# Performance work log

Measured on AMD Instinct MI355X. Metric: run time of the kernel, lower is better.

The kernel has to match this reference:

```python
import jax, jax.numpy as jnp
import numpy as np


def setup_inputs() -> dict:
    key = jax.random.key(0)
    k1, k2 = jax.random.split(key)
    x = jax.random.normal(k1, (65536, 256), dtype=jnp.float32)
    w = jax.random.normal(k2, (256, 1024), dtype=jnp.float32)
    return {"x": x, "w": w}


def reference(x, w):
    # out[b, u] = sum_f (x[b, f] - w[f, u])^2
    x_sq = jnp.sum(x * x, axis=1, keepdims=True)          # [B, 1]
    w_sq = jnp.sum(w * w, axis=0, keepdims=True)          # [1, U]
    cross = jnp.matmul(x, w)                               # [B, U]
    return x_sq - 2.0 * cross + w_sq
```

## Files before the change

### kernel.cpp

```cpp
#include <hip/hip_runtime.h>
#include <stdint.h>

#define M_DIM 65536
#define N_DIM 1024
#define K_DIM 256
#define BM 128
#define BN 128
#define BK 64

typedef __attribute__((ext_vector_type(8))) short short8;
typedef __attribute__((ext_vector_type(8))) unsigned short ushort8;
typedef __attribute__((ext_vector_type(16))) float float16;

__device__ __forceinline__ unsigned short f2bf(float f) {
    unsigned u = __builtin_bit_cast(unsigned, f);
    u += 0x7FFFu + ((u >> 16) & 1u);
    return (unsigned short)(u >> 16);
}

__global__ void prep_w(const float* __restrict__ w,
                       unsigned short* __restrict__ wT,
                       float* __restrict__ w_sq) {
    const int n = blockIdx.x * 256 + threadIdx.x;
    float sq = 0.f;
    for (int kc = 0; kc < 4; ++kc) {
        for (int c = 0; c < 8; ++c) {
            ushort8 pk;
            #pragma unroll
            for (int j = 0; j < 8; ++j) {
                float v = w[(size_t)(kc * 64 + c * 8 + j) * N_DIM + n];
                sq += v * v;
                pk[j] = f2bf(-2.0f * v);
            }
            *(ushort8*)(&wT[kc * 65536 + n * 64 + ((c ^ (n & 7)) << 3)]) = pk;
        }
    }
    w_sq[n] = sq;
}

__global__ __launch_bounds__(256, 3)
void gemm_rbf(const float* __restrict__ x,
              const unsigned short* __restrict__ wT,
              const float* __restrict__ w_sq,
              float* __restrict__ out) {
    __shared__ unsigned short xs[BM * BK];
    __shared__ unsigned short ws[BN * BK];
    __shared__ float xsq_p[16][132];
    __shared__ float xsq[BM];

    const int tid  = threadIdx.x;
    const int lane = tid & 63;
    const int wave = tid >> 6;
    const int wy = wave >> 1, wx = wave & 1;
    const int l31 = lane & 31;
    const int lhi = lane >> 5;
    const int bid = blockIdx.x;
    const int m0 = (bid >> 3) * BM;
    const int n0 = (bid & 7) * BN;

    float16 acc[2][2];
    #pragma unroll
    for (int ty = 0; ty < 2; ++ty)
        #pragma unroll
        for (int tx = 0; tx < 2; ++tx)
            #pragma unroll
            for (int i = 0; i < 16; ++i) acc[ty][tx][i] = 0.f;

    float xpart[8];
    #pragma unroll
    for (int p = 0; p < 8; ++p) xpart[p] = 0.f;

    const int xr = tid >> 4;
    const int xc = tid & 15;

    for (int kt = 0; kt < 4; ++kt) {
        __syncthreads();
        {
            const uint4* __restrict__ src = (const uint4*)(wT + (size_t)kt * 65536 + (size_t)n0 * 64);
            uint4* dst = (uint4*)ws;
            #pragma unroll
            for (int i = 0; i < 4; ++i) dst[tid * 4 + i] = src[tid * 4 + i];
        }
        {
            #pragma unroll
            for (int p = 0; p < 8; ++p) {
                const int r = xr + p * 16;
                const float4 v = *(const float4*)(x + (size_t)(m0 + r) * K_DIM + kt * BK + xc * 4);
                xpart[p] += v.x * v.x + v.y * v.y + v.z * v.z + v.w * v.w;
                uint2 pk;
                pk.x = (unsigned)f2bf(v.x) | ((unsigned)f2bf(v.y) << 16);
                pk.y = (unsigned)f2bf(v.z) | ((unsigned)f2bf(v.w) << 16);
                char* dst = (char*)xs + r * 128 + (((xc >> 1) ^ (r & 7)) << 4) + ((xc & 1) << 3);
                *(uint2*)dst = pk;
            }
        }
        __syncthreads();
        const int arow0 = wy * 64 + l31;
        const int bcol0 = wx * 64 + l31;
        #pragma unroll
        for (int ks = 0; ks < 4; ++ks) {
            const int c = ks * 2 + lhi;
            short8 a[2], b[2];
            #pragma unroll
            for (int ty = 0; ty < 2; ++ty) {
                const int r = arow0 + ty * 32;
                a[ty] = *(const short8*)((const char*)xs + r * 128 + ((c ^ (r & 7)) << 4));
            }
            #pragma unroll
            for (int tx = 0; tx < 2; ++tx) {
                const int cc = bcol0 + tx * 32;
                b[tx] = *(const short8*)((const char*)ws + cc * 128 + ((c ^ (cc & 7)) << 4));
            }
            #pragma unroll
            for (int ty = 0; ty < 2; ++ty)
                #pragma unroll
                for (int tx = 0; tx < 2; ++tx)
                    acc[ty][tx] = __builtin_amdgcn_mfma_f32_32x32x16_bf16(
                        a[ty], b[tx], acc[ty][tx], 0, 0, 0);
        }
    }

    #pragma unroll
    for (int p = 0; p < 8; ++p) xsq_p[xc][xr + p * 16] = xpart[p];
    __syncthreads();
    if (tid < BM) {
        float s = 0.f;
        #pragma unroll
        for (int c = 0; c < 16; ++c) s += xsq_p[c][tid];
        xsq[tid] = s;
    }
    __syncthreads();

    float wsqv[2];
    #pragma unroll
    for (int tx = 0; tx < 2; ++tx) wsqv[tx] = w_sq[n0 + wx * 64 + tx * 32 + l31];

    #pragma unroll
    for (int ty = 0; ty < 2; ++ty) {
        const int rbase = wy * 64 + ty * 32 + 4 * lhi;
        float xv[16];
        #pragma unroll
        for (int i = 0; i < 16; ++i) xv[i] = xsq[rbase + (i & 3) + 8 * (i >> 2)];
        #pragma unroll
        for (int tx = 0; tx < 2; ++tx) {
            const int col = n0 + wx * 64 + tx * 32 + l31;
            #pragma unroll
            for (int i = 0; i < 16; ++i) {
                const int row = m0 + rbase + (i & 3) + 8 * (i >> 2);
                out[(size_t)row * N_DIM + col] = xv[i] + acc[ty][tx][i] + wsqv[tx];
            }
        }
    }
}

__global__ void fallback_k(const float* __restrict__ x, const float* __restrict__ w,
                           float* __restrict__ out) {
    __shared__ float xrow[K_DIM];
    const int b = blockIdx.x;
    xrow[threadIdx.x] = x[(size_t)b * K_DIM + threadIdx.x];
    __syncthreads();
    for (int g = 0; g < 4; ++g) {
        const int u = g * 256 + threadIdx.x;
        float s = 0.f;
        for (int k = 0; k < K_DIM; ++k) {
            const float d = xrow[k] - w[(size_t)k * N_DIM + u];
            s += d * d;
        }
        out[(size_t)b * N_DIM + u] = s;
    }
}

extern "C" void kernel_launch(void* const* d_in, const int* in_sizes, int n_in,
                              void* d_out, int out_size, void* d_ws, size_t ws_size,
                              hipStream_t stream) {
    const float* x = (const float*)d_in[0];
    const float* w = (const float*)d_in[1];
    float* out = (float*)d_out;

    const size_t wT_bytes = (size_t)4 * 1024 * 64 * 2;
    const size_t need = wT_bytes + N_DIM * sizeof(float);
    if (ws_size < need) {
        fallback_k<<<M_DIM, 256, 0, stream>>>(x, w, out);
        return;
    }
    unsigned short* wT = (unsigned short*)d_ws;
    float* w_sq = (float*)((char*)d_ws + wT_bytes);

    prep_w<<<4, 256, 0, stream>>>(w, wT, w_sq);
    gemm_rbf<<<(M_DIM / BM) * (N_DIM / BN), 256, 0, stream>>>(x, wT, w_sq, out);
}
```

Measured before the change: 475.6 us.

## Fuse weight prep into GEMM, prefetch x tiles, and remap blocks per XCD

Removes the separate prep_w kernel. Each GEMM block now loads fp32 w directly, converts it to bf16 scaled by -2, and computes the w column norms in-kernel. The x tile for the next k-step is prefetched into registers while the current one is processed, and the x-norm reduction uses wave shuffles instead of shared memory. The block index is remapped so consecutive blocks on an XCD share m rows. This removes one launch and the serialized prep kernel, at the cost of redundant w conversion in each of the many blocks and higher register pressure.

```diff
diff --git a/kernel.cpp b/kernel.cpp
--- a/kernel.cpp
+++ b/kernel.cpp
@@ -9,44 +9,22 @@
 #define BK 64
 
 typedef __attribute__((ext_vector_type(8))) short short8;
-typedef __attribute__((ext_vector_type(8))) unsigned short ushort8;
 typedef __attribute__((ext_vector_type(16))) float float16;
 
-__device__ __forceinline__ unsigned short f2bf(float f) {
+__device__ __forceinline__ unsigned f2bf(float f) {
     unsigned u = __builtin_bit_cast(unsigned, f);
     u += 0x7FFFu + ((u >> 16) & 1u);
-    return (unsigned short)(u >> 16);
-}
-
-__global__ void prep_w(const float* __restrict__ w,
-                       unsigned short* __restrict__ wT,
-                       float* __restrict__ w_sq) {
-    const int n = blockIdx.x * 256 + threadIdx.x;
-    float sq = 0.f;
-    for (int kc = 0; kc < 4; ++kc) {
-        for (int c = 0; c < 8; ++c) {
-            ushort8 pk;
-            #pragma unroll
-            for (int j = 0; j < 8; ++j) {
-                float v = w[(size_t)(kc * 64 + c * 8 + j) * N_DIM + n];
-                sq += v * v;
-                pk[j] = f2bf(-2.0f * v);
-            }
-            *(ushort8*)(&wT[kc * 65536 + n * 64 + ((c ^ (n & 7)) << 3)]) = pk;
-        }
-    }
-    w_sq[n] = sq;
+    return u >> 16;
 }
 
 __global__ __launch_bounds__(256, 3)
 void gemm_rbf(const float* __restrict__ x,
-              const unsigned short* __restrict__ wT,
-              const float* __restrict__ w_sq,
+              const float* __restrict__ w,
               float* __restrict__ out) {
     __shared__ unsigned short xs[BM * BK];
     __shared__ unsigned short ws[BN * BK];
-    __shared__ float xsq_p[16][132];
     __shared__ float xsq[BM];
+    __shared__ float wsq_p[2][BN];
 
     const int tid  = threadIdx.x;
     const int lane = tid & 63;
@@ -54,9 +32,12 @@
     const int wy = wave >> 1, wx = wave & 1;
     const int l31 = lane & 31;
     const int lhi = lane >> 5;
+
     const int bid = blockIdx.x;
-    const int m0 = (bid >> 3) * BM;
-    const int n0 = (bid & 7) * BN;
+    const int xcd = bid & 7;
+    const int idx = bid >> 3;
+    const int n0 = (idx & 7) * BN;
+    const int m0 = ((xcd << 6) + (idx >> 3)) * BM;
 
     float16 acc[2][2];
     #pragma unroll
@@ -69,32 +50,59 @@
     float xpart[8];
     #pragma unroll
     for (int p = 0; p < 8; ++p) xpart[p] = 0.f;
+    float wsq_r = 0.f;
 
     const int xr = tid >> 4;
     const int xc = tid & 15;
+    const int wcol = tid & 127;
+    const int wkh  = tid >> 7;
+
+    float4 xv[8];
+    #pragma unroll
+    for (int p = 0; p < 8; ++p)
+        xv[p] = *(const float4*)(x + (size_t)(m0 + xr + p * 16) * K_DIM + xc * 4);
 
     for (int kt = 0; kt < 4; ++kt) {
+        float wv[4][8];
+        #pragma unroll
+        for (int c = 0; c < 4; ++c)
+            #pragma unroll
+            for (int j = 0; j < 8; ++j)
+                wv[c][j] = w[(size_t)(kt * BK + wkh * 32 + c * 8 + j) * N_DIM + n0 + wcol];
+
         __syncthreads();
-        {
-            const uint4* __restrict__ src = (const uint4*)(wT + (size_t)kt * 65536 + (size_t)n0 * 64);
-            uint4* dst = (uint4*)ws;
+
+        #pragma unroll
+        for (int p = 0; p < 8; ++p) {
+            const int r = xr + p * 16;
+            const float4 v = xv[p];
+            xpart[p] += v.x * v.x + v.y * v.y + v.z * v.z + v.w * v.w;
+            uint2 pk;
+            pk.x = f2bf(v.x) | (f2bf(v.y) << 16);
+            pk.y = f2bf(v.z) | (f2bf(v.w) << 16);
+            *(uint2*)((char*)xs + r * 128 + (((xc >> 1) ^ (r & 7)) << 4) + ((xc & 1) << 3)) = pk;
+        }
+
+        if (kt < 3) {
             #pragma unroll
-            for (int i = 0; i < 4; ++i) dst[tid * 4 + i] = src[tid * 4 + i];
+            for (int p = 0; p < 8; ++p)
+                xv[p] = *(const float4*)(x + (size_t)(m0 + xr + p * 16) * K_DIM + (kt + 1) * BK + xc * 4);
         }
-        {
+
+        #pragma unroll
+        for (int c = 0; c < 4; ++c) {
+            short8 pk;
             #pragma unroll
-            for (int p = 0; p < 8; ++p) {
-                const int r = xr + p * 16;
-                const float4 v = *(const float4*)(x + (size_t)(m0 + r) * K_DIM + kt * BK + xc * 4);
-                xpart[p] += v.x * v.x + v.y * v.y + v.z * v.z + v.w * v.w;
-                uint2 pk;
-                pk.x = (unsigned)f2bf(v.x) | ((unsigned)f2bf(v.y) << 16);
-                pk.y = (unsigned)f2bf(v.z) | ((unsigned)f2bf(v.w) << 16);
-                char* dst = (char*)xs + r * 128 + (((xc >> 1) ^ (r & 7)) << 4) + ((xc & 1) << 3);
-                *(uint2*)dst = pk;
+            for (int j = 0; j < 8; ++j) {
+                const float v = wv[c][j];
+                wsq_r += v * v;
+                pk[j] = (short)f2bf(-2.0f * v);
             }
+            *(short8*)((char*)ws + wcol * 128 + (((wkh * 4 + c) ^ (wcol & 7)) << 4)) = pk;
         }
+
         __syncthreads();
+
         const int arow0 = wy * 64 + l31;
         const int bcol0 = wx * 64 + l31;
         #pragma unroll
@@ -121,52 +129,39 @@
     }
 
     #pragma unroll
-    for (int p = 0; p < 8; ++p) xsq_p[xc][xr + p * 16] = xpart[p];
-    __syncthreads();
-    if (tid < BM) {
-        float s = 0.f;
-        #pragma unroll
-        for (int c = 0; c < 16; ++c) s += xsq_p[c][tid];
-        xsq[tid] = s;
+    for (int p = 0; p < 8; ++p) {
+        float s = xpart[p];
+        s += __shfl_xor(s, 1);
+        s += __shfl_xor(s, 2);
+        s += __shfl_xor(s, 4);
+        s += __shfl_xor(s, 8);
+        if (xc == 0) xsq[xr + p * 16] = s;
     }
+    wsq_p[wkh][wcol] = wsq_r;
     __syncthreads();
 
     float wsqv[2];
     #pragma unroll
-    for (int tx = 0; tx < 2; ++tx) wsqv[tx] = w_sq[n0 + wx * 64 + tx * 32 + l31];
+    for (int tx = 0; tx < 2; ++tx) {
+        const int c = wx * 64 + tx * 32 + l31;
+        wsqv[tx] = wsq_p[0][c] + wsq_p[1][c];
+    }
 
     #pragma unroll
     for (int ty = 0; ty < 2; ++ty) {
         const int rbase = wy * 64 + ty * 32 + 4 * lhi;
-        float xv[16];
+        float xvv[16];
         #pragma unroll
-        for (int i = 0; i < 16; ++i) xv[i] = xsq[rbase + (i & 3) + 8 * (i >> 2)];
+        for (int i = 0; i < 16; ++i) xvv[i] = xsq[rbase + (i & 3) + 8 * (i >> 2)];
         #pragma unroll
         for (int tx = 0; tx < 2; ++tx) {
             const int col = n0 + wx * 64 + tx * 32 + l31;
             #pragma unroll
             for (int i = 0; i < 16; ++i) {
                 const int row = m0 + rbase + (i & 3) + 8 * (i >> 2);
-                out[(size_t)row * N_DIM + col] = xv[i] + acc[ty][tx][i] + wsqv[tx];
+                out[(size_t)row * N_DIM + col] = xvv[i] + acc[ty][tx][i] + wsqv[tx];
             }
         }
-    }
-}
-
-__global__ void fallback_k(const float* __restrict__ x, const float* __restrict__ w,
-                           float* __restrict__ out) {
-    __shared__ float xrow[K_DIM];
-    const int b = blockIdx.x;
-    xrow[threadIdx.x] = x[(size_t)b * K_DIM + threadIdx.x];
-    __syncthreads();
-    for (int g = 0; g < 4; ++g) {
-        const int u = g * 256 + threadIdx.x;
-        float s = 0.f;
-        for (int k = 0; k < K_DIM; ++k) {
-            const float d = xrow[k] - w[(size_t)k * N_DIM + u];
-            s += d * d;
-        }
-        out[(size_t)b * N_DIM + u] = s;
     }
 }
 
@@ -176,16 +171,7 @@
     const float* x = (const float*)d_in[0];
     const float* w = (const float*)d_in[1];
     float* out = (float*)d_out;
+    (void)d_ws; (void)ws_size;
 
-    const size_t wT_bytes = (size_t)4 * 1024 * 64 * 2;
-    const size_t need = wT_bytes + N_DIM * sizeof(float);
-    if (ws_size < need) {
-        fallback_k<<<M_DIM, 256, 0, stream>>>(x, w, out);
-        return;
-    }
-    unsigned short* wT = (unsigned short*)d_ws;
-    float* w_sq = (float*)((char*)d_ws + wT_bytes);
-
-    prep_w<<<4, 256, 0, stream>>>(w, wT, w_sq);
-    gemm_rbf<<<(M_DIM / BM) * (N_DIM / BN), 256, 0, stream>>>(x, wT, w_sq, out);
+    gemm_rbf<<<(M_DIM / BM) * (N_DIM / BN), 256, 0, stream>>>(x, w, out);
 }
```

Result: slower. 829.6 us (+74.4%).
